# Kernel optimization log

Measured on AMD Instinct MI355X. Metric: run time of the kernel, lower is better.

The kernel has to match this reference:

```python
import jax, jax.numpy as jnp
import numpy as np

B, S = 1, 2048
D = 4096          # hidden_size
H, HK, DH = 32, 8, 128  # num_heads, num_kv_heads, head_dim
THETA = 10000.0


def setup_inputs() -> dict:
    key = jax.random.key(0)
    k0, k1, k2, k3, k4 = jax.random.split(key, 5)
    std = 0.02
    return {
        "position_ids": jnp.broadcast_to(jnp.arange(S, dtype=jnp.int32), (B, S)),
        "hidden_states": jax.random.normal(k0, (B, S, D), jnp.float32),
        "Wq": (jax.random.normal(k1, (D, H * DH), jnp.float32) * std),
        "Wk": (jax.random.normal(k2, (D, HK * DH), jnp.float32) * std),
        "Wv": (jax.random.normal(k3, (D, HK * DH), jnp.float32) * std),
        "Wo": (jax.random.normal(k4, (H * DH, D), jnp.float32) * std),
    }


def _rope(x, pos):
    """Neox-style rotary embedding over the full head_dim. x: [B,S,h,DH]."""
    half = DH // 2
    inv_freq = 1.0 / (THETA ** (jnp.arange(half, dtype=jnp.float32) * 2.0 / DH))
    ang = pos[..., None].astype(jnp.float32) * inv_freq          # [B,S,half]
    cos = jnp.cos(ang)[:, :, None, :]
    sin = jnp.sin(ang)[:, :, None, :]
    x1, x2 = x[..., :half], x[..., half:]
    return jnp.concatenate([x1 * cos - x2 * sin, x2 * cos + x1 * sin], axis=-1)


def reference(position_ids, hidden_states, Wq, Wk, Wv, Wo):
    q = (hidden_states @ Wq).reshape(B, S, H, DH)
    k = (hidden_states @ Wk).reshape(B, S, HK, DH)
    v = (hidden_states @ Wv).reshape(B, S, HK, DH)
    q = _rope(q, position_ids)
    k = _rope(k, position_ids)

    G = H // HK  # query heads per kv head (GQA)
    qg = q.reshape(B, S, HK, G, DH)
    scale = jnp.float32(DH) ** -0.5
    scores = jnp.einsum('bqhgd,bkhd->bhgqk', qg, k) * scale      # [B,HK,G,S,S]
    causal = jnp.tril(jnp.ones((S, S), dtype=bool))
    scores = jnp.where(causal, scores, jnp.finfo(scores.dtype).min)
    p = jax.nn.softmax(scores, axis=-1)
    out = jnp.einsum('bhgqk,bkhd->bqhgd', p, v).reshape(B, S, H * DH)
    return out @ Wo
```

## Files before the change

kernel.cpp:

```cpp
#include <hip/hip_runtime.h>

typedef unsigned short u16;
typedef short bf16x8 __attribute__((ext_vector_type(8)));
typedef float f32x4 __attribute__((ext_vector_type(4)));

#define GLB __attribute__((address_space(1)))
#define LDSAS __attribute__((address_space(3)))

constexpr int S = 2048, D = 4096, NH = 32, NHK = 8, DHD = 128;
constexpr int NQKV = 6144;

__device__ __forceinline__ u16 f2b(float f) {
    union { float f; unsigned u; } v; v.f = f;
    return (u16)((v.u + 0x7fffu + ((v.u >> 16) & 1u)) >> 16);
}
__device__ __forceinline__ float b2f(u16 b) {
    union { unsigned u; float f; } v; v.u = ((unsigned)b) << 16;
    return v.f;
}
__device__ __forceinline__ void gload16(const void* g, void* l) {
    __builtin_amdgcn_global_load_lds((const GLB unsigned int*)g,
                                     (LDSAS unsigned int*)l, 16, 0, 0);
}
#if __has_builtin(__builtin_amdgcn_exp2f)
__device__ __forceinline__ float exp2fast(float x) { return __builtin_amdgcn_exp2f(x); }
#else
__device__ __forceinline__ float exp2fast(float x) { return __expf(0.6931471805599453f * x); }
#endif

__device__ __forceinline__ void sincos_big(float ang, float* sn, float* cs) {
#if __has_builtin(__builtin_amdgcn_sinf) && __has_builtin(__builtin_amdgcn_cosf)
    float rev = ang * 0.15915494309189535f;
    rev = rev - floorf(rev);
    *sn = __builtin_amdgcn_sinf(rev);
    *cs = __builtin_amdgcn_cosf(rev);
#else
    *sn = sinf(ang);
    *cs = cosf(ang);
#endif
}

__global__ __launch_bounds__(256) void cvt_x(const float* __restrict__ in,
                                             u16* __restrict__ out, int n8) {
    int i = blockIdx.x * 256 + threadIdx.x;
    if (i >= n8) return;
    const float4* p = (const float4*)in + (size_t)i * 2;
    float4 a = p[0], b = p[1];
    uint4 o;
    o.x = f2b(a.x) | ((unsigned)f2b(a.y) << 16);
    o.y = f2b(a.z) | ((unsigned)f2b(a.w) << 16);
    o.z = f2b(b.x) | ((unsigned)f2b(b.y) << 16);
    o.w = f2b(b.z) | ((unsigned)f2b(b.w) << 16);
    *(uint4*)(out + (size_t)i * 8) = o;
}

__global__ __launch_bounds__(256) void tconv(const float* __restrict__ in,
                                             u16* __restrict__ out, int R, int C) {
    __shared__ float t[64][65];
    int r0 = blockIdx.y * 64, c0 = blockIdx.x * 64;
    int tx = threadIdx.x & 63, ty = threadIdx.x >> 6;
#pragma unroll
    for (int i = 0; i < 64; i += 4)
        t[ty + i][tx] = in[(size_t)(r0 + ty + i) * C + c0 + tx];
    __syncthreads();
#pragma unroll
    for (int i = 0; i < 64; i += 4)
        out[(size_t)(c0 + ty + i) * R + r0 + tx] = f2b(t[tx][ty + i]);
}

__global__ __launch_bounds__(256) void vtrans(const u16* __restrict__ QKV,
                                              u16* __restrict__ Vt) {
    __shared__ u16 t[64][65];
    int hk = blockIdx.z;
    int s0 = blockIdx.x * 64, d0 = blockIdx.y * 64;
    int tx = threadIdx.x & 63, ty = threadIdx.x >> 6;
#pragma unroll
    for (int i = 0; i < 64; i += 4)
        t[ty + i][tx] = QKV[(size_t)(s0 + ty + i) * NQKV + 5120 + hk * 128 + d0 + tx];
    __syncthreads();
#pragma unroll
    for (int i = 0; i < 64; i += 4)
        Vt[(size_t)hk * (128 * 2048) + (size_t)(d0 + ty + i) * 2048 + s0 + tx] = t[tx][ty + i];
}

template <int NHEADS>
__global__ __launch_bounds__(256) void rope2(u16* __restrict__ T,
                                             const int* __restrict__ pos, float scale) {
    int idx = blockIdx.x * 256 + threadIdx.x;
    int d = idx & 63;
    int h = (idx >> 6) & (NHEADS - 1);
    int s = idx >> (6 + (NHEADS == 32 ? 5 : 3));
    float p = (float)pos[s];
    float inv = __expf(-(float)d * 0.14391156531310576f);
    float ang = p * inv;
    float sn, cs;
    sincos_big(ang, &sn, &cs);
    size_t base = (size_t)s * NQKV + h * 128 + d;
    float x1 = b2f(T[base]), x2 = b2f(T[base + 64]);
    T[base]      = f2b((x1 * cs - x2 * sn) * scale);
    T[base + 64] = f2b((x2 * cs + x1 * sn) * scale);
}

template <bool BF16OUT>
__global__ __launch_bounds__(512, 2) void gemm256(const u16* __restrict__ A,
                                                  const u16* __restrict__ Bt,
                                                  void* __restrict__ Cout,
                                                  int N, int K, int nbx) {
    __shared__ u16 Asm[2][256 * 64];
    __shared__ u16 Bsm[2][256 * 64];
    const int cpx = (int)gridDim.x >> 3;
    const int b = ((int)blockIdx.x & 7) * cpx + ((int)blockIdx.x >> 3);
    const int by = b / nbx, bx = b - by * nbx;
    const int m0 = by * 256, n0 = bx * 256;
    const int tid = threadIdx.x;
    const int lane = tid & 63, wave = tid >> 6;
    const int l15 = lane & 15, l4 = lane >> 4;
    const int wm = wave >> 2, wn = wave & 3;
    f32x4 acc[8][4] = {};

    auto stageA = [&](int t, int buf, int h) {
#pragma unroll
        for (int u = 0; u < 2; ++u) {
            int s = u * 512 + tid;
            int row = s >> 3;
            int cs = (s & 7) ^ (row & 7);
            gload16(A + (size_t)(m0 + h * 128 + row) * K + t * 64 + cs * 8,
                    &Asm[buf][h * 8192 + s * 8]);
        }
    };
    auto stageB = [&](int t, int buf, int h) {
#pragma unroll
        for (int u = 0; u < 2; ++u) {
            int s = u * 512 + tid;
            int row = s >> 3;
            int cs = (s & 7) ^ (row & 7);
            gload16(Bt + (size_t)(n0 + h * 128 + row) * K + t * 64 + cs * 8,
                    &Bsm[buf][h * 8192 + s * 8]);
        }
    };

    const int NT = K >> 6;
    stageA(0, 0, 0); stageA(0, 0, 1); stageB(0, 0, 0); stageB(0, 0, 1);
    asm volatile("s_waitcnt vmcnt(0)" ::: "memory");
    __builtin_amdgcn_s_barrier();

    bf16x8 af[4][2], bf0[2][2], bf1[2][2];
#pragma unroll 1
    for (int t = 0; t < NT; ++t) {
        const int c = t & 1;
        const bool pre = (t + 1 < NT);
#pragma unroll
        for (int i = 0; i < 4; ++i)
#pragma unroll
            for (int kk = 0; kk < 2; ++kk) {
                int row = wm * 128 + i * 16 + l15;
                int cc = (kk * 4 + l4) ^ (row & 7);
                af[i][kk] = *(const bf16x8*)(&Asm[c][row * 64 + cc * 8]);
            }
#pragma unroll
        for (int j = 0; j < 2; ++j)
#pragma unroll
            for (int kk = 0; kk < 2; ++kk) {
                int row = wn * 64 + j * 16 + l15;
                int cc = (kk * 4 + l4) ^ (row & 7);
                bf0[j][kk] = *(const bf16x8*)(&Bsm[c][row * 64 + cc * 8]);
            }
        if (pre) { stageA(t + 1, c ^ 1, 0); stageA(t + 1, c ^ 1, 1); }
        __builtin_amdgcn_s_barrier();
        asm volatile("s_waitcnt lgkmcnt(0)" ::: "memory");
        __builtin_amdgcn_s_setprio(1);
#pragma unroll
        for (int i = 0; i < 4; ++i)
#pragma unroll
            for (int j = 0; j < 2; ++j)
#pragma unroll
                for (int kk = 0; kk < 2; ++kk)
                    acc[i][j] = __builtin_amdgcn_mfma_f32_16x16x32_bf16(af[i][kk], bf0[j][kk], acc[i][j], 0, 0, 0);
        __builtin_amdgcn_s_setprio(0);
        __builtin_amdgcn_s_barrier();
#pragma unroll
        for (int j = 0; j < 2; ++j)
#pragma unroll
            for (int kk = 0; kk < 2; ++kk) {
                int row = wn * 64 + (j + 2) * 16 + l15;
                int cc = (kk * 4 + l4) ^ (row & 7);
                bf1[j][kk] = *(const bf16x8*)(&Bsm[c][row * 64 + cc * 8]);
            }
        if (pre) { stageB(t + 1, c ^ 1, 0); stageB(t + 1, c ^ 1, 1); }
        __builtin_amdgcn_s_barrier();
        asm volatile("s_waitcnt lgkmcnt(0)" ::: "memory");
        __builtin_amdgcn_s_setprio(1);
#pragma unroll
        for (int i = 0; i < 4; ++i)
#pragma unroll
            for (int j = 0; j < 2; ++j)
#pragma unroll
                for (int kk = 0; kk < 2; ++kk)
                    acc[i][j + 2] = __builtin_amdgcn_mfma_f32_16x16x32_bf16(af[i][kk], bf1[j][kk], acc[i][j + 2], 0, 0, 0);
        __builtin_amdgcn_s_setprio(0);
        __builtin_amdgcn_s_barrier();
#pragma unroll
        for (int i = 0; i < 4; ++i)
#pragma unroll
            for (int kk = 0; kk < 2; ++kk) {
                int row = wm * 128 + (i + 4) * 16 + l15;
                int cc = (kk * 4 + l4) ^ (row & 7);
                af[i][kk] = *(const bf16x8*)(&Asm[c][row * 64 + cc * 8]);
            }
        __builtin_amdgcn_s_barrier();
        asm volatile("s_waitcnt lgkmcnt(0)" ::: "memory");
        __builtin_amdgcn_s_setprio(1);
#pragma unroll
        for (int i = 0; i < 4; ++i)
#pragma unroll
            for (int j = 0; j < 2; ++j)
#pragma unroll
                for (int kk = 0; kk < 2; ++kk)
                    acc[i + 4][j] = __builtin_amdgcn_mfma_f32_16x16x32_bf16(af[i][kk], bf0[j][kk], acc[i + 4][j], 0, 0, 0);
        __builtin_amdgcn_s_setprio(0);
        __builtin_amdgcn_s_barrier();
        __builtin_amdgcn_s_setprio(1);
#pragma unroll
        for (int i = 0; i < 4; ++i)
#pragma unroll
            for (int j = 0; j < 2; ++j)
#pragma unroll
                for (int kk = 0; kk < 2; ++kk)
                    acc[i + 4][j + 2] = __builtin_amdgcn_mfma_f32_16x16x32_bf16(af[i][kk], bf1[j][kk], acc[i + 4][j + 2], 0, 0, 0);
        __builtin_amdgcn_s_setprio(0);
        asm volatile("s_waitcnt vmcnt(0)" ::: "memory");
        __builtin_amdgcn_s_barrier();
    }
#pragma unroll
    for (int i = 0; i < 8; ++i)
#pragma unroll
        for (int j = 0; j < 4; ++j) {
            int col  = n0 + wn * 64 + j * 16 + l15;
            int rowb = m0 + wm * 128 + i * 16 + l4 * 4;
#pragma unroll
            for (int r = 0; r < 4; ++r) {
                if (BF16OUT)
                    ((u16*)Cout)[(size_t)(rowb + r) * N + col] = f2b(acc[i][j][r]);
                else
                    ((float*)Cout)[(size_t)(rowb + r) * N + col] = acc[i][j][r];
            }
        }
}

__global__ __launch_bounds__(256) void attn3(const u16* __restrict__ QKV,
                                             const u16* __restrict__ Vt,
                                             u16* __restrict__ O) {
    __shared__ u16 Ksm[2][64 * 128];
    __shared__ u16 Vsm[2][128 * 64];
    __shared__ u16 Psm[4][16 * 64];
    const int orig = blockIdx.x;
    const int swz = (orig & 7) * 64 + (orig >> 3);
    const int h = swz >> 4, p = swz & 15;
    const int hk = h >> 2;
    const int tid = threadIdx.x, wave = tid >> 6, lane = tid & 63;
    const int l15 = lane & 15, l4 = lane >> 4;
    const u16* Qp = QKV + h * 128;
    const u16* Kp = QKV + 4096 + hk * 128;
    const u16* Vp = Vt + (size_t)hk * (128 * 2048);

    auto stage = [&](int kb, int b) {
#pragma unroll
        for (int it = 0; it < 4; ++it) {
            int L = it * 256 + tid;
            int krow = L >> 4, kslot = L & 15;
            int kcs = (kslot & 8) | ((kslot ^ krow) & 7);
            gload16(Kp + (size_t)(kb * 64 + krow) * NQKV + kcs * 8, &Ksm[b][L * 8]);
            int vrow = L >> 3, vslot = L & 7;
            int vcs = (vslot ^ vrow) & 7;
            gload16(Vp + (size_t)vrow * 2048 + kb * 64 + vcs * 8, &Vsm[b][L * 8]);
        }
    };

#pragma unroll 1
    for (int pass = 0; pass < 2; ++pass) {
        const int qt = pass ? p : 31 - p;
        const int qr0 = qt * 64 + wave * 16;
        const int nkb = qt + 1;

        bf16x8 qf[4];
        {
            const u16* qrow = Qp + (size_t)(qr0 + l15) * NQKV;
#pragma unroll
            for (int c = 0; c < 4; ++c)
                qf[c] = *(const bf16x8*)(qrow + c * 32 + l4 * 8);
        }
        float mrow[4], lsum[4];
#pragma unroll
        for (int r = 0; r < 4; ++r) { mrow[r] = -1e30f; lsum[r] = 0.f; }
        f32x4 o[8] = {};

        stage(0, 0);
#pragma unroll 1
        for (int kb = 0; kb < nkb; ++kb) {
            const int cur = kb & 1;
            if (kb + 1 < nkb) {
                stage(kb + 1, cur ^ 1);
                asm volatile("s_waitcnt vmcnt(8)" ::: "memory");
            } else {
                asm volatile("s_waitcnt vmcnt(0)" ::: "memory");
            }
            __builtin_amdgcn_s_barrier();

            if (kb * 64 <= qr0 + 15) {
                const u16* Kb_ = Ksm[cur];
                const u16* Vb_ = Vsm[cur];
                const bool diag = (kb * 64 + 63 > qr0);
                f32x4 sc[4] = {};
#pragma unroll
                for (int f = 0; f < 4; ++f) {
                    const int kv = f * 16 + l15;
#pragma unroll
                    for (int c = 0; c < 4; ++c) {
                        int cd = c * 4 + l4;
                        int cpos = (cd & 8) | ((cd ^ kv) & 7);
                        bf16x8 kf = *(const bf16x8*)(Kb_ + kv * 128 + cpos * 8);
                        sc[f] = __builtin_amdgcn_mfma_f32_16x16x32_bf16(qf[c], kf, sc[f], 0, 0, 0);
                    }
                }
                if (diag) {
#pragma unroll
                    for (int f = 0; f < 4; ++f) {
                        int col = kb * 64 + f * 16 + l15;
#pragma unroll
                        for (int r = 0; r < 4; ++r) {
                            int row = qr0 + l4 * 4 + r;
                            if (col > row) sc[f][r] = -1e30f;
                        }
                    }
                }
                float bm[4];
#pragma unroll
                for (int r = 0; r < 4; ++r)
                    bm[r] = fmaxf(fmaxf(sc[0][r], sc[1][r]), fmaxf(sc[2][r], sc[3][r]));
#pragma unroll
                for (int msk = 1; msk < 16; msk <<= 1)
#pragma unroll
                    for (int r = 0; r < 4; ++r) bm[r] = fmaxf(bm[r], __shfl_xor(bm[r], msk));

                bool need = false;
#pragma unroll
                for (int r = 0; r < 4; ++r) need = need || (bm[r] > mrow[r] + 8.0f);
                if (__any((int)need)) {
                    float al[4];
#pragma unroll
                    for (int r = 0; r < 4; ++r) {
                        float mn = fmaxf(mrow[r], bm[r]);
                        al[r] = exp2fast(mrow[r] - mn);
                        mrow[r] = mn;
                        lsum[r] *= al[r];
                    }
#pragma unroll
                    for (int n = 0; n < 8; ++n)
#pragma unroll
                        for (int r = 0; r < 4; ++r) o[n][r] *= al[r];
                }
                float rs[4] = {0.f, 0.f, 0.f, 0.f};
#pragma unroll
                for (int f = 0; f < 4; ++f) {
#pragma unroll
                    for (int r = 0; r < 4; ++r) {
                        float pw = exp2fast(sc[f][r] - mrow[r]);
                        rs[r] += pw;
                        int q = l4 * 4 + r;
                        int kvc = f * 2 + (l15 >> 3);
                        int slot = (kvc ^ q) & 7;
                        Psm[wave][q * 64 + slot * 8 + (l15 & 7)] = f2b(pw);
                    }
                }
#pragma unroll
                for (int msk = 1; msk < 16; msk <<= 1)
#pragma unroll
                    for (int r = 0; r < 4; ++r) rs[r] += __shfl_xor(rs[r], msk);
#pragma unroll
                for (int r = 0; r < 4; ++r) lsum[r] += rs[r];

                asm volatile("s_waitcnt lgkmcnt(0)" ::: "memory");
                bf16x8 pf[2];
#pragma unroll
                for (int c = 0; c < 2; ++c) {
                    int chc = c * 4 + l4;
                    int slot = (chc ^ l15) & 7;
                    pf[c] = *(const bf16x8*)(&Psm[wave][l15 * 64 + slot * 8]);
                }
#pragma unroll
                for (int n = 0; n < 8; ++n) {
                    int d = n * 16 + l15;
                    bf16x8 vf[2];
#pragma unroll
                    for (int c = 0; c < 2; ++c) {
                        int ch = c * 4 + l4;
                        int slot = (ch ^ d) & 7;
                        vf[c] = *(const bf16x8*)(Vb_ + d * 64 + slot * 8);
                    }
#pragma unroll
                    for (int c = 0; c < 2; ++c)
                        o[n] = __builtin_amdgcn_mfma_f32_16x16x32_bf16(pf[c], vf[c], o[n], 0, 0, 0);
                }
            }
            asm volatile("s_waitcnt lgkmcnt(0)" ::: "memory");
            __builtin_amdgcn_s_barrier();
        }

        float inv[4];
#pragma unroll
        for (int r = 0; r < 4; ++r) inv[r] = 1.0f / lsum[r];
#pragma unroll
        for (int n = 0; n < 8; ++n)
#pragma unroll
            for (int r = 0; r < 4; ++r) {
                int row = qr0 + l4 * 4 + r;
                O[(size_t)row * 4096 + h * 128 + n * 16 + l15] = f2b(o[n][r] * inv[r]);
            }
    }
}

extern "C" void kernel_launch(void* const* d_in, const int* in_sizes, int n_in,
                              void* d_out, int out_size, void* d_ws, size_t ws_size,
                              hipStream_t stream) {
    const int*   pos = (const int*)d_in[0];
    const float* X   = (const float*)d_in[1];
    const float* Wq  = (const float*)d_in[2];
    const float* Wk  = (const float*)d_in[3];
    const float* Wv  = (const float*)d_in[4];
    const float* Wo  = (const float*)d_in[5];
    float* out = (float*)d_out;

    char* w = (char*)d_ws;
    u16* Xb    = (u16*)(w + 0);
    u16* Wqkvt = (u16*)(w + 16777216);
    u16* Wot   = (u16*)(w + 67108864);
    u16* QKV   = (u16*)(w + 100663296);
    u16* Vtb   = (u16*)(w + 125829120);
    u16* Ob    = (u16*)(w + 130023424);

    const float SC2 = 0.08838834764831845f * 1.4426950408889634f;

    cvt_x<<<4096, 256, 0, stream>>>(X, Xb, S * D / 8);
    tconv<<<dim3(64, 64), 256, 0, stream>>>(Wq, Wqkvt, 4096, 4096);
    tconv<<<dim3(16, 64), 256, 0, stream>>>(Wk, Wqkvt + (size_t)4096 * 4096, 4096, 1024);
    tconv<<<dim3(16, 64), 256, 0, stream>>>(Wv, Wqkvt + (size_t)5120 * 4096, 4096, 1024);
    tconv<<<dim3(64, 64), 256, 0, stream>>>(Wo, Wot, 4096, 4096);

    gemm256<true><<<192, 512, 0, stream>>>(Xb, Wqkvt, QKV, NQKV, 4096, 24);

    rope2<32><<<16384, 256, 0, stream>>>(QKV, pos, SC2);
    rope2<8><<<4096, 256, 0, stream>>>(QKV + 4096, pos, 1.0f);

    vtrans<<<dim3(32, 2, 8), 256, 0, stream>>>(QKV, Vtb);

    attn3<<<512, 256, 0, stream>>>(QKV, Vtb, Ob);

    gemm256<false><<<128, 512, 0, stream>>>(Ob, Wot, out, 4096, 4096, 16);
}
```

Before: 389.8 us.

## Use narrower GEMM N-tiles for more blocks and pipeline loads with partial vmcnt waits

```diff
diff --git a/kernel.cpp b/kernel.cpp
--- a/kernel.cpp
+++ b/kernel.cpp
@@ -6,6 +6,7 @@
 
 #define GLB __attribute__((address_space(1)))
 #define LDSAS __attribute__((address_space(3)))
+#define WAITV(n) asm volatile("s_waitcnt vmcnt(" #n ")" ::: "memory")
 
 constexpr int S = 2048, D = 4096, NH = 32, NHK = 8, DHD = 128;
 constexpr int NQKV = 6144;
@@ -101,111 +102,115 @@
     T[base + 64] = f2b((x2 * cs + x1 * sn) * scale);
 }
 
-template <bool BF16OUT>
-__global__ __launch_bounds__(512, 2) void gemm256(const u16* __restrict__ A,
-                                                  const u16* __restrict__ Bt,
-                                                  void* __restrict__ Cout,
-                                                  int N, int K, int nbx) {
+template <int BN, bool BF16OUT>
+__global__ __launch_bounds__(512, 2) void gemmP(const u16* __restrict__ A,
+                                                const u16* __restrict__ Bt,
+                                                void* __restrict__ Cout,
+                                                int N, int K) {
+    constexpr int NJ = BN / 64;
+    constexpr int NBU = BN / 64;
+    constexpr int WCOL = BN / 4;
     __shared__ u16 Asm[2][256 * 64];
-    __shared__ u16 Bsm[2][256 * 64];
+    __shared__ u16 Bsm[2][BN * 64];
     const int cpx = (int)gridDim.x >> 3;
     const int b = ((int)blockIdx.x & 7) * cpx + ((int)blockIdx.x >> 3);
+    const int nbx = N / BN;
     const int by = b / nbx, bx = b - by * nbx;
-    const int m0 = by * 256, n0 = bx * 256;
-    const int tid = threadIdx.x;
-    const int lane = tid & 63, wave = tid >> 6;
+    const int m0 = by * 256, n0 = bx * BN;
+    const int tid = threadIdx.x, lane = tid & 63, wave = tid >> 6;
     const int l15 = lane & 15, l4 = lane >> 4;
     const int wm = wave >> 2, wn = wave & 3;
-    f32x4 acc[8][4] = {};
-
-    auto stageA = [&](int t, int buf, int h) {
+    f32x4 acc[8][NJ] = {};
+
+    auto stA = [&](int t, int buf, int half) {
 #pragma unroll
         for (int u = 0; u < 2; ++u) {
             int s = u * 512 + tid;
-            int row = s >> 3;
-            int cs = (s & 7) ^ (row & 7);
-            gload16(A + (size_t)(m0 + h * 128 + row) * K + t * 64 + cs * 8,
-                    &Asm[buf][h * 8192 + s * 8]);
+            int row = s >> 3, cs = (s & 7) ^ (row & 7);
+            gload16(A + (size_t)(m0 + half * 128 + row) * K + t * 64 + cs * 8,
+                    &Asm[buf][half * 8192 + s * 8]);
         }
     };
-    auto stageB = [&](int t, int buf, int h) {
-#pragma unroll
-        for (int u = 0; u < 2; ++u) {
-            int s = u * 512 + tid;
-            int row = s >> 3;
-            int cs = (s & 7) ^ (row & 7);
-            gload16(Bt + (size_t)(n0 + h * 128 + row) * K + t * 64 + cs * 8,
-                    &Bsm[buf][h * 8192 + s * 8]);
-        }
+    auto stB1 = [&](int t, int buf, int u0) {
+        int row = u0 * 64 + (tid >> 3);
+        int cs = (tid & 7) ^ (row & 7);
+        gload16(Bt + (size_t)(n0 + row) * K + t * 64 + cs * 8,
+                &Bsm[buf][u0 * 4096 + tid * 8]);
     };
 
     const int NT = K >> 6;
-    stageA(0, 0, 0); stageA(0, 0, 1); stageB(0, 0, 0); stageB(0, 0, 1);
-    asm volatile("s_waitcnt vmcnt(0)" ::: "memory");
+    stA(0, 0, 0);
+#pragma unroll
+    for (int u = 0; u < NBU; ++u) stB1(0, 0, u);
+    stA(0, 0, 1);
+    WAITV(2);
     __builtin_amdgcn_s_barrier();
 
-    bf16x8 af[4][2], bf0[2][2], bf1[2][2];
+    bf16x8 af[4][2], bf[NJ][2];
 #pragma unroll 1
     for (int t = 0; t < NT; ++t) {
-        const int c = t & 1;
+        const int cur = t & 1, nxt = cur ^ 1;
         const bool pre = (t + 1 < NT);
+        const u16* Ab = &Asm[cur][0];
+        const u16* Bb = &Bsm[cur][0];
 #pragma unroll
         for (int i = 0; i < 4; ++i)
 #pragma unroll
             for (int kk = 0; kk < 2; ++kk) {
-                int row = wm * 128 + i * 16 + l15;
+                int row = wm * 64 + i * 16 + l15;
                 int cc = (kk * 4 + l4) ^ (row & 7);
-                af[i][kk] = *(const bf16x8*)(&Asm[c][row * 64 + cc * 8]);
-            }
-#pragma unroll
-        for (int j = 0; j < 2; ++j)
+                af[i][kk] = *(const bf16x8*)(Ab + row * 64 + cc * 8);
+            }
+#pragma unroll
+        for (int j = 0; j < NJ - 1; ++j)
 #pragma unroll
             for (int kk = 0; kk < 2; ++kk) {
-                int row = wn * 64 + j * 16 + l15;
+                int row = wn * WCOL + j * 16 + l15;
                 int cc = (kk * 4 + l4) ^ (row & 7);
-                bf0[j][kk] = *(const bf16x8*)(&Bsm[c][row * 64 + cc * 8]);
-            }
-        if (pre) { stageA(t + 1, c ^ 1, 0); stageA(t + 1, c ^ 1, 1); }
+                bf[j][kk] = *(const bf16x8*)(Bb + row * 64 + cc * 8);
+            }
+        if (pre) stA(t + 1, nxt, 0);
         __builtin_amdgcn_s_barrier();
         asm volatile("s_waitcnt lgkmcnt(0)" ::: "memory");
         __builtin_amdgcn_s_setprio(1);
 #pragma unroll
         for (int i = 0; i < 4; ++i)
 #pragma unroll
-            for (int j = 0; j < 2; ++j)
+            for (int j = 0; j < NJ - 1; ++j)
 #pragma unroll
                 for (int kk = 0; kk < 2; ++kk)
-                    acc[i][j] = __builtin_amdgcn_mfma_f32_16x16x32_bf16(af[i][kk], bf0[j][kk], acc[i][j], 0, 0, 0);
+                    acc[i][j] = __builtin_amdgcn_mfma_f32_16x16x32_bf16(af[i][kk], bf[j][kk], acc[i][j], 0, 0, 0);
         __builtin_amdgcn_s_setprio(0);
         __builtin_amdgcn_s_barrier();
 #pragma unroll
-        for (int j = 0; j < 2; ++j)
-#pragma unroll
-            for (int kk = 0; kk < 2; ++kk) {
-                int row = wn * 64 + (j + 2) * 16 + l15;
-                int cc = (kk * 4 + l4) ^ (row & 7);
-                bf1[j][kk] = *(const bf16x8*)(&Bsm[c][row * 64 + cc * 8]);
-            }
-        if (pre) { stageB(t + 1, c ^ 1, 0); stageB(t + 1, c ^ 1, 1); }
+        for (int kk = 0; kk < 2; ++kk) {
+            int row = wn * WCOL + (NJ - 1) * 16 + l15;
+            int cc = (kk * 4 + l4) ^ (row & 7);
+            bf[NJ - 1][kk] = *(const bf16x8*)(Bb + row * 64 + cc * 8);
+        }
+        if (pre) {
+#pragma unroll
+            for (int u = 0; u < NBU; ++u) stB1(t + 1, nxt, u);
+        }
         __builtin_amdgcn_s_barrier();
         asm volatile("s_waitcnt lgkmcnt(0)" ::: "memory");
         __builtin_amdgcn_s_setprio(1);
 #pragma unroll
         for (int i = 0; i < 4; ++i)
 #pragma unroll
-            for (int j = 0; j < 2; ++j)
-#pragma unroll
-                for (int kk = 0; kk < 2; ++kk)
-                    acc[i][j + 2] = __builtin_amdgcn_mfma_f32_16x16x32_bf16(af[i][kk], bf1[j][kk], acc[i][j + 2], 0, 0, 0);
+            for (int kk = 0; kk < 2; ++kk)
+                acc[i][NJ - 1] = __builtin_amdgcn_mfma_f32_16x16x32_bf16(af[i][kk], bf[NJ - 1][kk], acc[i][NJ - 1], 0, 0, 0);
         __builtin_amdgcn_s_setprio(0);
+        if (pre) { if constexpr (NBU == 3) WAITV(5); else WAITV(4); }
+        else WAITV(0);
         __builtin_amdgcn_s_barrier();
 #pragma unroll
         for (int i = 0; i < 4; ++i)
 #pragma unroll
             for (int kk = 0; kk < 2; ++kk) {
-                int row = wm * 128 + (i + 4) * 16 + l15;
+                int row = wm * 64 + i * 16 + l15;
                 int cc = (kk * 4 + l4) ^ (row & 7);
-                af[i][kk] = *(const bf16x8*)(&Asm[c][row * 64 + cc * 8]);
+                af[i][kk] = *(const bf16x8*)(Ab + 8192 + row * 64 + cc * 8);
             }
         __builtin_amdgcn_s_barrier();
         asm volatile("s_waitcnt lgkmcnt(0)" ::: "memory");
@@ -213,30 +218,29 @@
 #pragma unroll
         for (int i = 0; i < 4; ++i)
 #pragma unroll
-            for (int j = 0; j < 2; ++j)
+            for (int j = 0; j < NJ - 1; ++j)
 #pragma unroll
                 for (int kk = 0; kk < 2; ++kk)
-                    acc[i + 4][j] = __builtin_amdgcn_mfma_f32_16x16x32_bf16(af[i][kk], bf0[j][kk], acc[i + 4][j], 0, 0, 0);
+                    acc[i + 4][j] = __builtin_amdgcn_mfma_f32_16x16x32_bf16(af[i][kk], bf[j][kk], acc[i + 4][j], 0, 0, 0);
         __builtin_amdgcn_s_setprio(0);
         __builtin_amdgcn_s_barrier();
+        if (pre) stA(t + 1, nxt, 1);
         __builtin_amdgcn_s_setprio(1);
 #pragma unroll
         for (int i = 0; i < 4; ++i)
 #pragma unroll
-            for (int j = 0; j < 2; ++j)
-#pragma unroll
-                for (int kk = 0; kk < 2; ++kk)
-                    acc[i + 4][j + 2] = __builtin_amdgcn_mfma_f32_16x16x32_bf16(af[i][kk], bf1[j][kk], acc[i + 4][j + 2], 0, 0, 0);
+            for (int kk = 0; kk < 2; ++kk)
+                acc[i + 4][NJ - 1] = __builtin_amdgcn_mfma_f32_16x16x32_bf16(af[i][kk], bf[NJ - 1][kk], acc[i + 4][NJ - 1], 0, 0, 0);
         __builtin_amdgcn_s_setprio(0);
-        asm volatile("s_waitcnt vmcnt(0)" ::: "memory");
+        if (pre) WAITV(2);
         __builtin_amdgcn_s_barrier();
     }
 #pragma unroll
     for (int i = 0; i < 8; ++i)
 #pragma unroll
-        for (int j = 0; j < 4; ++j) {
-            int col  = n0 + wn * 64 + j * 16 + l15;
-            int rowb = m0 + wm * 128 + i * 16 + l4 * 4;
+        for (int j = 0; j < NJ; ++j) {
+            int col = n0 + wn * WCOL + j * 16 + l15;
+            int rowb = m0 + (i < 4 ? wm * 64 + i * 16 : 128 + wm * 64 + (i - 4) * 16) + l4 * 4;
 #pragma unroll
             for (int r = 0; r < 4; ++r) {
                 if (BF16OUT)
@@ -446,7 +450,7 @@
     tconv<<<dim3(16, 64), 256, 0, stream>>>(Wv, Wqkvt + (size_t)5120 * 4096, 4096, 1024);
     tconv<<<dim3(64, 64), 256, 0, stream>>>(Wo, Wot, 4096, 4096);
 
-    gemm256<true><<<192, 512, 0, stream>>>(Xb, Wqkvt, QKV, NQKV, 4096, 24);
+    gemmP<192, true><<<256, 512, 0, stream>>>(Xb, Wqkvt, QKV, NQKV, 4096);
 
     rope2<32><<<16384, 256, 0, stream>>>(QKV, pos, SC2);
     rope2<8><<<4096, 256, 0, stream>>>(QKV + 4096, pos, 1.0f);
@@ -455,5 +459,5 @@
 
     attn3<<<512, 256, 0, stream>>>(QKV, Vtb, Ob);
 
-    gemm256<false><<<128, 512, 0, stream>>>(Ob, Wot, out, 4096, 4096, 16);
-}
+    gemmP<128, false><<<256, 512, 0, stream>>>(Ob, Wot, out, 4096, 4096);
+}
```

Result: no change. 396.4 us (+1.7%).
